# Optimization experiments

Measured on AMD Instinct MI355X. Metric: run time of the kernel, lower is better.

The kernel has to match this reference:

```python
import jax, jax.numpy as jnp
import numpy as np

# ---- model constants (match init_kwargs) ----
B, N, T, L = 16384, 32, 300, 1
DIM = 2                      # len(state_index)
DT = 1.0 / (T * L)           # dt = 1/(T*l)
STEPS = T * L                # Euler integration steps (time_steps = STEPS+1)
A_X = 1.0                    # canonical DMP phase constant
TAU = 1.0
HID = 64
OUT = N * DIM + DIM          # fc2_mean output size


def setup_inputs() -> dict:
    key = jax.random.key(0)
    ks = jax.random.split(key, 8)
    s = lambda i, shape, scale: jax.random.normal(ks[i], shape, jnp.float32) * scale
    inp = {
        "state": jax.random.normal(ks[0], (B, 3), jnp.float32),
        "fc1_w": s(1, (HID, 3), 0.3),
        "fc1_b": jnp.full((HID,), 0.1, jnp.float32),
        "fc2m_w": s(2, (OUT, HID), 0.1),
        "fc2m_b": jnp.full((OUT,), 0.1, jnp.float32),
        "sig_w": s(3, (DIM, HID), 0.1),
        "sig_b": jnp.zeros((DIM,), jnp.float32),
        "val_w": s(4, (DIM, HID), 0.1),
        "val_b": jnp.zeros((DIM,), jnp.float32),
    }
    # DMPParameters: gaussian RBF centers on exp-decayed phase, canonical widths
    c = jnp.exp(-A_X * jnp.linspace(0.0, 1.0, N))
    inp["dmp_c"] = c.astype(jnp.float32)
    inp["dmp_sigma2"] = (N ** 1.5 / c / A_X).astype(jnp.float32)
    return inp


def dmp_rollout(w, goal, y0, dy0, a_z, c, sigma2):
    """Euler rollout of DMP transformation system.
    w: [M,N] basis weights, goal/y0/dy0/a_z: [M] per-channel scalars.
    Returns Y, dY, ddY each [M, STEPS+1]."""
    z0 = dy0 * TAU
    b_z = a_z / 4.0

    def step(carry, _):
        x, y, z = carry
        x = x + (-A_X * x) * TAU * DT                       # phase update
        psi = jnp.exp(-0.5 * (x - c) ** 2 / sigma2)          # [N] gaussian RBF
        fx = (w @ psi) * x * (goal - y0) / jnp.sum(psi)      # [M] forcing term
        dz = a_z * (b_z * (goal - y) - z) + fx
        dy = z
        y = y + TAU * dy * DT
        z = z + TAU * dz * DT
        return (x, y, z), (y, dy * TAU, dz * TAU)

    _, (Ys, dYs, ddYs) = jax.lax.scan(
        step, (jnp.float32(1.0), y0, z0), None, length=STEPS)
    Y = jnp.concatenate([y0[None], Ys], axis=0).T            # [M, STEPS+1]
    dY = jnp.concatenate([dy0[None], dYs], axis=0).T
    ddY = jnp.concatenate([z0[None], ddYs], axis=0).T
    return Y, dY, ddY


def reference(state, fc1_w, fc1_b, fc2m_w, fc2m_b, sig_w, sig_b,
              val_w, val_b, dmp_c, dmp_sigma2):
    x = jnp.tanh(state @ fc1_w.T + fc1_b) * 0.1              # [B,64]
    y0 = state[:, :DIM].reshape(-1)                           # [M=B*DIM]
    dy0 = jnp.zeros_like(y0) + 0.01

    # value = fc2_value(x).repeat(1,T).view(-1,T,2).transpose(1,2) == broadcast over T
    v = x @ val_w.T + val_b                                   # [B,2]
    value = jnp.broadcast_to(v[:, :, None], (B, DIM, T))

    sigma = (jax.nn.sigmoid(x @ sig_w.T + sig_b) * 1.0 + 0.001).reshape(-1, DIM, 1)

    ndp_wg = x @ fc2m_w.T + fc2m_b                            # [B, 2N+2]
    goal = ndp_wg[:, :DIM].reshape(-1)                        # [M]
    w = ndp_wg[:, DIM:DIM * (N + 1)].reshape(-1, N)           # [M,N]
    a_z = jnp.clip(ndp_wg[:, -1], 0.5, 30.0)                  # learned a_z (az=True)
    a_z = jnp.broadcast_to(a_z[:, None], (B, DIM)).reshape(-1)

    Y, _, _ = dmp_rollout(w, goal, y0, dy0, a_z, dmp_c, dmp_sigma2)
    y = Y.reshape(B, DIM, -1)[:, :, ::L]                      # [B,2,T+1]
    a = y[:, :, 1:] - y[:, :, :-1]                            # [B,2,T]
    return (a, sigma, value)
```

## Files before the change

kernel.cpp:

```cpp
#include <hip/hip_runtime.h>
#include <hip/hip_bf16.h>

#define NB 32
#define TS 300
#define NBATCH 16384
#define DTF (1.0f/300.0f)
#define A_ELEMS (NBATCH*2*TS)

typedef __attribute__((ext_vector_type(8))) short bf16x8;
typedef __attribute__((ext_vector_type(4))) float f32x4;

static __device__ __forceinline__ ushort f2bf(float f) {
    union { __hip_bfloat16 h; ushort u; } cv;
    cv.h = __float2bfloat16(f);
    return cv.u;
}


__global__ __launch_bounds__(256) void k_head(
    const float* __restrict__ state,
    const float* __restrict__ fc1_w, const float* __restrict__ fc1_b,
    const float* __restrict__ fc2m_w, const float* __restrict__ fc2m_b,
    const float* __restrict__ sig_w, const float* __restrict__ sig_b,
    const float* __restrict__ val_w, const float* __restrict__ val_b,
    const float* __restrict__ dmp_c, const float* __restrict__ dmp_s2,
    float* __restrict__ sig_out, float* __restrict__ pbuf,
    ushort* __restrict__ wbuf16, uint4* __restrict__ wsPhi)
{
    const int tid = threadIdx.x;
    if (blockIdx.x == 256) {
        const float l2 = log2f(1.0f - DTF);
        for (int t = tid; t < 304; t += 256) {
            ushort row[NB];
            if (t < TS) {
                const float x = exp2f((float)(t + 1) * l2);
                float ps[NB]; float s = 0.0f;
                #pragma unroll
                for (int n = 0; n < NB; ++n) {
                    float d = x - dmp_c[n];
                    float p = __expf(-0.5f * d * d / dmp_s2[n]);
                    ps[n] = p; s += p;
                }
                const float inv = x / s;
                #pragma unroll
                for (int n = 0; n < NB; ++n) row[n] = f2bf(ps[n] * inv);
            } else {
                #pragma unroll
                for (int n = 0; n < NB; ++n) row[n] = 0;
            }
            #pragma unroll
            for (int g0 = 0; g0 < 4; ++g0) {
                union { ushort us[8]; uint4 v; } pk;
                #pragma unroll
                for (int e = 0; e < 8; ++e) pk.us[e] = row[g0*8 + e];
                wsPhi[(t >> 4)*64 + g0*16 + (t & 15)] = pk.v;
            }
        }
        return;
    }

    __shared__ uint4 bfr[640];
    __shared__ float f1s[64*4];
    __shared__ float biasl[80];
    __shared__ float hlds[4*16*68];
    __shared__ float ct[4*16*84];
    __shared__ float scl[4][16][2];

    const int wv  = tid >> 6;
    const int l   = tid & 63;
    const int b16 = l & 15;
    const int g   = l >> 4;

    for (int e = tid; e < 640; e += 256) {
        const int T = e >> 7, kk = (e >> 6) & 1, lane = e & 63;
        const int r = T*16 + (lane & 15);
        const int k0 = kk*32 + (lane >> 4)*8;
        union { ushort us[8]; uint4 v; } pk;
        if (r < 70) {
            const float* src = (r < 66) ? (fc2m_w + r*64 + k0)
                             : (r < 68) ? (sig_w + (r-66)*64 + k0)
                             : (val_w + (r-68)*64 + k0);
            #pragma unroll
            for (int i = 0; i < 8; ++i) pk.us[i] = f2bf(src[i]);
        } else {
            #pragma unroll
            for (int i = 0; i < 8; ++i) pk.us[i] = 0;
        }
        bfr[e] = pk.v;
    }
    if (tid < 64) {
        f1s[tid*4+0] = fc1_w[tid*3+0];
        f1s[tid*4+1] = fc1_w[tid*3+1];
        f1s[tid*4+2] = fc1_w[tid*3+2];
        f1s[tid*4+3] = fc1_b[tid];
    }
    if (tid < 80) biasl[tid] = (tid < 66) ? fc2m_b[tid] : (tid < 68) ? sig_b[tid-66]
                             : (tid < 70) ? val_b[tid-68] : 0.0f;
    __syncthreads();

    const int bbase = blockIdx.x*64 + wv*16;
    const int bglob = bbase + b16;
    const float s0 = state[bglob*3+0], s1 = state[bglob*3+1], s2 = state[bglob*3+2];

    float* hrow = hlds + wv*1088 + b16*68;
    #pragma unroll
    for (int i = 0; i < 16; ++i) {
        const int hid = g + 4*i;
        const float4 fw = *(const float4*)(f1s + hid*4);
        const float pre = fmaf(fw.x, s0, fmaf(fw.y, s1, fmaf(fw.z, s2, fw.w)));
        const float e = __expf(2.0f * pre);
        hrow[hid] = (1.0f - 2.0f/(e + 1.0f)) * 0.1f;
    }

    bf16x8 A0, A1;
    {
        const float* hr = hlds + wv*1088 + b16*68 + g*8;
        const float4 h0 = *(const float4*)(hr),      h1 = *(const float4*)(hr + 4);
        const float4 h2 = *(const float4*)(hr + 32), h3 = *(const float4*)(hr + 36);
        union { bf16x8 v; ushort u[8]; } p0, p1;
        p0.u[0]=f2bf(h0.x); p0.u[1]=f2bf(h0.y); p0.u[2]=f2bf(h0.z); p0.u[3]=f2bf(h0.w);
        p0.u[4]=f2bf(h1.x); p0.u[5]=f2bf(h1.y); p0.u[6]=f2bf(h1.z); p0.u[7]=f2bf(h1.w);
        p1.u[0]=f2bf(h2.x); p1.u[1]=f2bf(h2.y); p1.u[2]=f2bf(h2.z); p1.u[3]=f2bf(h2.w);
        p1.u[4]=f2bf(h3.x); p1.u[5]=f2bf(h3.y); p1.u[6]=f2bf(h3.z); p1.u[7]=f2bf(h3.w);
        A0 = p0.v; A1 = p1.v;
    }

    float* ctw = ct + wv*1344;
    const f32x4 zacc = {0.0f, 0.0f, 0.0f, 0.0f};
    #pragma unroll
    for (int T = 0; T < 5; ++T) {
        union { uint4 q; bf16x8 v; } B0, B1;
        B0.q = bfr[(T*2+0)*64 + l];
        B1.q = bfr[(T*2+1)*64 + l];
        f32x4 acc = __builtin_amdgcn_mfma_f32_16x16x32_bf16(A0, B0.v, zacc, 0, 0, 0);
        acc = __builtin_amdgcn_mfma_f32_16x16x32_bf16(A1, B1.v, acc, 0, 0, 0);
        const int r = T*16 + b16;
        const float bs = biasl[r];
        #pragma unroll
        for (int reg = 0; reg < 4; ++reg)
            ctw[(g*4 + reg)*84 + r] = acc[reg] + bs;
    }

    if (l < 32) {
        const int b = l & 15, d = l >> 4;
        const float goal = ctw[b*84 + d];
        const float y0 = state[(bbase + b)*3 + d];
        scl[wv][b][d] = DTF * (goal - y0);
    }

    uint* wout = (uint*)wbuf16;
    #pragma unroll 1
    for (int b = 0; b < 16; ++b) {
        if (l < 32) {
            const float2 wp = *(const float2*)(ctw + b*84 + 2 + 2*l);
            const float sc = scl[wv][b][l >> 4];
            wout[(bbase + b)*32 + l] =
                (uint)f2bf(wp.x * sc) | ((uint)f2bf(wp.y * sc) << 16);
        }
    }
    if (l < 16) {
        const float* cb = ctw + l*84;
        const float az = fminf(fmaxf(cb[65], 0.5f), 30.0f);
        const float y0 = state[(bbase + l)*3 + 0];
        *(float4*)(pbuf + ((bbase + l)*2 + 0)*4) = make_float4(cb[0], az, y0, cb[68]);
    } else if (l < 32) {
        const int b = l - 16;
        const float* cb = ctw + b*84;
        const float az = fminf(fmaxf(cb[65], 0.5f), 30.0f);
        const float y0 = state[(bbase + b)*3 + 1];
        *(float4*)(pbuf + ((bbase + b)*2 + 1)*4) = make_float4(cb[1], az, y0, cb[69]);
    } else if (l < 48) {
        const int b = l - 32;
        const float* cb = ctw + b*84;
        const float sg0 = 1.0f / (1.0f + __expf(-cb[66])) + 0.001f;
        const float sg1 = 1.0f / (1.0f + __expf(-cb[67])) + 0.001f;
        *(float2*)(sig_out + (bbase + b)*2) = make_float2(sg0, sg1);
    }
}

__global__ __launch_bounds__(384) void k_roll(
    const uint4* __restrict__ wsPhi, const float* __restrict__ pbuf,
    const ushort* __restrict__ wbuf16, float* __restrict__ a_out,
    float* __restrict__ v_out)
{
    const int tid = threadIdx.x;
    const int wv = tid >> 6;
    const int l  = tid & 63;

    if (wv >= 4) {
        const int vw = wv - 4;
        const int mbase = (blockIdx.x << 6) + (vw << 5);
        #pragma unroll 1
        for (int r = 0; r < 32; ++r) {
            const int mch = mbase + r;
            const float fv = pbuf[mch*4 + 3];
            float4* vrow = (float4*)(v_out + mch*TS);
            const float4 vq = make_float4(fv, fv, fv, fv);
            vrow[l] = vq;
            if (l < 11) vrow[64 + l] = vq;
        }
        return;
    }

    const int ch = l & 15;
    const int g  = l >> 4;
    const int m  = (blockIdx.x << 6) + (wv << 4) + ch;

    const float4 pp = *(const float4*)(pbuf + m*4);
    const float az = pp.y;
    const float Ac = (DTF * 0.25f) * az * az;
    const float OmB = fmaf(-DTF, az, 1.0f);
    const float c0 = Ac * pp.x;
    float y = pp.z;
    float z = 0.01f;
    const f32x4 cvec = {c0, c0, c0, c0};

    const bf16x8 wb = *(const bf16x8*)(wbuf16 + m*NB + g*8);
    const bf16x8* ap = (const bf16x8*)wsPhi;
    bf16x8 af = ap[l];

    float* aptr = a_out + m*TS + (g << 2);

    for (int c = 0; c < 19; ++c) {
        f32x4 facc = __builtin_amdgcn_mfma_f32_16x16x32_bf16(af, wb, cvec, 0, 0, 0);
        if (c < 18) af = ap[(c + 1)*64 + l];

        float F[16];
        #pragma unroll
        for (int q = 0; q < 4; ++q) {
            float a = facc[q], b = facc[q];
            asm volatile("v_permlane16_swap_b32 %0, %1" : "+v"(a), "+v"(b));
            float a2 = a, b2 = b;
            asm volatile("v_permlane32_swap_b32 %0, %1" : "+v"(a), "+v"(a2));
            asm volatile("v_permlane32_swap_b32 %0, %1" : "+v"(b), "+v"(b2));
            F[0*4+q] = a; F[1*4+q] = b; F[2*4+q] = a2; F[3*4+q] = b2;
        }

        float avq[4];
        #pragma unroll
        for (int i = 0; i < 16; ++i) {
            const float t2 = fmaf(-Ac, y, F[i]);
            if (g == (i >> 2)) avq[i & 3] = z;
            y = fmaf(DTF, z, y);
            z = fmaf(OmB, z, t2);
        }

        if ((c < 18) | (g < 3)) {
            *(float4*)aptr = make_float4(avq[0]*DTF, avq[1]*DTF, avq[2]*DTF, avq[3]*DTF);
        }
        aptr += 16;
    }
}

extern "C" void kernel_launch(void* const* d_in, const int* in_sizes, int n_in,
                              void* d_out, int out_size, void* d_ws, size_t ws_size,
                              hipStream_t stream) {
    (void)in_sizes; (void)n_in; (void)out_size; (void)ws_size;
    const float* state  = (const float*)d_in[0];
    const float* fc1_w  = (const float*)d_in[1];
    const float* fc1_b  = (const float*)d_in[2];
    const float* fc2m_w = (const float*)d_in[3];
    const float* fc2m_b = (const float*)d_in[4];
    const float* sig_w  = (const float*)d_in[5];
    const float* sig_b  = (const float*)d_in[6];
    const float* val_w  = (const float*)d_in[7];
    const float* val_b  = (const float*)d_in[8];
    const float* dmp_c  = (const float*)d_in[9];
    const float* dmp_s2 = (const float*)d_in[10];

    float* out     = (float*)d_out;
    float* a_out   = out;
    float* sig_out = out + A_ELEMS;
    float* v_out   = out + A_ELEMS + NBATCH*2;

    char* ws = (char*)d_ws;
    uint4*  wsPhi  = (uint4*)ws;
    float*  pbuf   = (float*)(ws + 32768);
    ushort* wbuf16 = (ushort*)(ws + 557056);

    k_head<<<dim3(257), dim3(256), 0, stream>>>(state, fc1_w, fc1_b, fc2m_w, fc2m_b,
                                                sig_w, sig_b, val_w, val_b,
                                                dmp_c, dmp_s2,
                                                sig_out, pbuf, wbuf16, wsPhi);
    k_roll<<<dim3(512), dim3(384), 0, stream>>>(wsPhi, pbuf, wbuf16, a_out, v_out);
}
```

Measured before the change: 27.96 us.

## Fuse head MLP and DMP rollout into one kernel with LDS-resident basis table

Merges the head kernel and the rollout kernel into a single 768-thread block. Each block computes the MLP head for its 64 batch rows, rebuilds the normalized RBF phase table in shared memory with two spare waves, and then runs the rollout and value broadcast for its own 128 channels after a block barrier. This removes the second kernel launch and the global round-trip of the basis table. In exchange every block recomputes the basis table, and the grid becomes 256 large blocks, which limits overlap and occupancy during the rollout.

After: 27.47 us. No clear change (-1.8%).

```diff
diff --git a/kernel.cpp b/kernel.cpp
--- a/kernel.cpp
+++ b/kernel.cpp
@@ -16,8 +16,7 @@
     return cv.u;
 }
 
-
-__global__ __launch_bounds__(256) void k_head(
+__global__ __launch_bounds__(768) void k_all(
     const float* __restrict__ state,
     const float* __restrict__ fc1_w, const float* __restrict__ fc1_b,
     const float* __restrict__ fc2m_w, const float* __restrict__ fc2m_b,
@@ -25,12 +24,50 @@
     const float* __restrict__ val_w, const float* __restrict__ val_b,
     const float* __restrict__ dmp_c, const float* __restrict__ dmp_s2,
     float* __restrict__ sig_out, float* __restrict__ pbuf,
-    ushort* __restrict__ wbuf16, uint4* __restrict__ wsPhi)
+    ushort* __restrict__ wbuf16,
+    float* __restrict__ a_out, float* __restrict__ v_out)
 {
+    __shared__ uint4 phiL[19*64];
+    __shared__ uint4 bfr[640];
+    __shared__ float f1s[64*4];
+    __shared__ float biasl[80];
+    __shared__ float hlds[4*16*68];
+    __shared__ float ct[4*16*84];
+    __shared__ float scl[4][16][2];
+
     const int tid = threadIdx.x;
-    if (blockIdx.x == 256) {
+    const int wv  = tid >> 6;
+    const int l   = tid & 63;
+
+    if (wv < 4) {
+        for (int e = tid; e < 640; e += 256) {
+            const int T = e >> 7, kk = (e >> 6) & 1, lane = e & 63;
+            const int r = T*16 + (lane & 15);
+            const int k0 = kk*32 + (lane >> 4)*8;
+            union { ushort us[8]; uint4 v; } pk;
+            if (r < 70) {
+                const float* src = (r < 66) ? (fc2m_w + r*64 + k0)
+                                 : (r < 68) ? (sig_w + (r-66)*64 + k0)
+                                 : (val_w + (r-68)*64 + k0);
+                #pragma unroll
+                for (int i = 0; i < 8; ++i) pk.us[i] = f2bf(src[i]);
+            } else {
+                #pragma unroll
+                for (int i = 0; i < 8; ++i) pk.us[i] = 0;
+            }
+            bfr[e] = pk.v;
+        }
+        if (tid < 64) {
+            f1s[tid*4+0] = fc1_w[tid*3+0];
+            f1s[tid*4+1] = fc1_w[tid*3+1];
+            f1s[tid*4+2] = fc1_w[tid*3+2];
+            f1s[tid*4+3] = fc1_b[tid];
+        }
+        if (tid < 80) biasl[tid] = (tid < 66) ? fc2m_b[tid] : (tid < 68) ? sig_b[tid-66]
+                                 : (tid < 70) ? val_b[tid-68] : 0.0f;
+    } else if (wv < 6) {
         const float l2 = log2f(1.0f - DTF);
-        for (int t = tid; t < 304; t += 256) {
+        for (int t = tid - 256; t < 304; t += 128) {
             ushort row[NB];
             if (t < TS) {
                 const float x = exp2f((float)(t + 1) * l2);
@@ -53,143 +90,148 @@
                 union { ushort us[8]; uint4 v; } pk;
                 #pragma unroll
                 for (int e = 0; e < 8; ++e) pk.us[e] = row[g0*8 + e];
-                wsPhi[(t >> 4)*64 + g0*16 + (t & 15)] = pk.v;
-            }
-        }
-        return;
+                phiL[(t >> 4)*64 + g0*16 + (t & 15)] = pk.v;
+            }
+        }
     }
-
-    __shared__ uint4 bfr[640];
-    __shared__ float f1s[64*4];
-    __shared__ float biasl[80];
-    __shared__ float hlds[4*16*68];
-    __shared__ float ct[4*16*84];
-    __shared__ float scl[4][16][2];
-
-    const int wv  = tid >> 6;
-    const int l   = tid & 63;
-    const int b16 = l & 15;
-    const int g   = l >> 4;
-
-    for (int e = tid; e < 640; e += 256) {
-        const int T = e >> 7, kk = (e >> 6) & 1, lane = e & 63;
-        const int r = T*16 + (lane & 15);
-        const int k0 = kk*32 + (lane >> 4)*8;
-        union { ushort us[8]; uint4 v; } pk;
-        if (r < 70) {
-            const float* src = (r < 66) ? (fc2m_w + r*64 + k0)
-                             : (r < 68) ? (sig_w + (r-66)*64 + k0)
-                             : (val_w + (r-68)*64 + k0);
-            #pragma unroll
-            for (int i = 0; i < 8; ++i) pk.us[i] = f2bf(src[i]);
-        } else {
-            #pragma unroll
-            for (int i = 0; i < 8; ++i) pk.us[i] = 0;
-        }
-        bfr[e] = pk.v;
+    __syncthreads();
+
+    if (wv < 4) {
+        const int b16 = l & 15;
+        const int g   = l >> 4;
+        const int bbase = blockIdx.x*64 + wv*16;
+        const int bglob = bbase + b16;
+        const float s0 = state[bglob*3+0], s1 = state[bglob*3+1], s2 = state[bglob*3+2];
+
+        float* hrow = hlds + wv*1088 + b16*68;
+        #pragma unroll
+        for (int i = 0; i < 16; ++i) {
+            const int hid = g + 4*i;
+            const float4 fw = *(const float4*)(f1s + hid*4);
+            const float pre = fmaf(fw.x, s0, fmaf(fw.y, s1, fmaf(fw.z, s2, fw.w)));
+            const float e = __expf(2.0f * pre);
+            hrow[hid] = (1.0f - 2.0f/(e + 1.0f)) * 0.1f;
+        }
+
+        bf16x8 A0, A1;
+        {
+            const float* hr = hlds + wv*1088 + b16*68 + g*8;
+            const float4 h0 = *(const float4*)(hr),      h1 = *(const float4*)(hr + 4);
+            const float4 h2 = *(const float4*)(hr + 32), h3 = *(const float4*)(hr + 36);
+            union { bf16x8 v; ushort u[8]; } p0, p1;
+            p0.u[0]=f2bf(h0.x); p0.u[1]=f2bf(h0.y); p0.u[2]=f2bf(h0.z); p0.u[3]=f2bf(h0.w);
+            p0.u[4]=f2bf(h1.x); p0.u[5]=f2bf(h1.y); p0.u[6]=f2bf(h1.z); p0.u[7]=f2bf(h1.w);
+            p1.u[0]=f2bf(h2.x); p1.u[1]=f2bf(h2.y); p1.u[2]=f2bf(h2.z); p1.u[3]=f2bf(h2.w);
+            p1.u[4]=f2bf(h3.x); p1.u[5]=f2bf(h3.y); p1.u[6]=f2bf(h3.z); p1.u[7]=f2bf(h3.w);
+            A0 = p0.v; A1 = p1.v;
+        }
+
+        float* ctw = ct + wv*1344;
+        const f32x4 zacc = {0.0f, 0.0f, 0.0f, 0.0f};
+        #pragma unroll
+        for (int T = 0; T < 5; ++T) {
+            union { uint4 q; bf16x8 v; } B0, B1;
+            B0.q = bfr[(T*2+0)*64 + l];
+            B1.q = bfr[(T*2+1)*64 + l];
+            f32x4 acc = __builtin_amdgcn_mfma_f32_16x16x32_bf16(A0, B0.v, zacc, 0, 0, 0);
+            acc = __builtin_amdgcn_mfma_f32_16x16x32_bf16(A1, B1.v, acc, 0, 0, 0);
+            const int r = T*16 + b16;
+            const float bs = biasl[r];
+            #pragma unroll
+            for (int reg = 0; reg < 4; ++reg)
+                ctw[(g*4 + reg)*84 + r] = acc[reg] + bs;
+        }
+
+        if (l < 32) {
+            const int b = l & 15, d = l >> 4;
+            const float goal = ctw[b*84 + d];
+            const float y0 = state[(bbase + b)*3 + d];
+            scl[wv][b][d] = DTF * (goal - y0);
+        }
+
+        uint* wout = (uint*)wbuf16;
+        #pragma unroll 1
+        for (int b = 0; b < 16; ++b) {
+            if (l < 32) {
+                const float2 wp = *(const float2*)(ctw + b*84 + 2 + 2*l);
+                const float sc = scl[wv][b][l >> 4];
+                wout[(bbase + b)*32 + l] =
+                    (uint)f2bf(wp.x * sc) | ((uint)f2bf(wp.y * sc) << 16);
+            }
+        }
+        if (l < 16) {
+            const float* cb = ctw + l*84;
+            const float az = fminf(fmaxf(cb[65], 0.5f), 30.0f);
+            const float y0 = state[(bbase + l)*3 + 0];
+            *(float4*)(pbuf + ((bbase + l)*2 + 0)*4) = make_float4(cb[0], az, y0, cb[68]);
+        } else if (l < 32) {
+            const int b = l - 16;
+            const float* cb = ctw + b*84;
+            const float az = fminf(fmaxf(cb[65], 0.5f), 30.0f);
+            const float y0 = state[(bbase + b)*3 + 1];
+            *(float4*)(pbuf + ((bbase + b)*2 + 1)*4) = make_float4(cb[1], az, y0, cb[69]);
+        } else if (l < 48) {
+            const int b = l - 32;
+            const float* cb = ctw + b*84;
+            const float sg0 = 1.0f / (1.0f + __expf(-cb[66])) + 0.001f;
+            const float sg1 = 1.0f / (1.0f + __expf(-cb[67])) + 0.001f;
+            *(float2*)(sig_out + (bbase + b)*2) = make_float2(sg0, sg1);
+        }
     }
-    if (tid < 64) {
-        f1s[tid*4+0] = fc1_w[tid*3+0];
-        f1s[tid*4+1] = fc1_w[tid*3+1];
-        f1s[tid*4+2] = fc1_w[tid*3+2];
-        f1s[tid*4+3] = fc1_b[tid];
-    }
-    if (tid < 80) biasl[tid] = (tid < 66) ? fc2m_b[tid] : (tid < 68) ? sig_b[tid-66]
-                             : (tid < 70) ? val_b[tid-68] : 0.0f;
     __syncthreads();
 
-    const int bbase = blockIdx.x*64 + wv*16;
-    const int bglob = bbase + b16;
-    const float s0 = state[bglob*3+0], s1 = state[bglob*3+1], s2 = state[bglob*3+2];
-
-    float* hrow = hlds + wv*1088 + b16*68;
-    #pragma unroll
-    for (int i = 0; i < 16; ++i) {
-        const int hid = g + 4*i;
-        const float4 fw = *(const float4*)(f1s + hid*4);
-        const float pre = fmaf(fw.x, s0, fmaf(fw.y, s1, fmaf(fw.z, s2, fw.w)));
-        const float e = __expf(2.0f * pre);
-        hrow[hid] = (1.0f - 2.0f/(e + 1.0f)) * 0.1f;
-    }
-
-    bf16x8 A0, A1;
-    {
-        const float* hr = hlds + wv*1088 + b16*68 + g*8;
-        const float4 h0 = *(const float4*)(hr),      h1 = *(const float4*)(hr + 4);
-        const float4 h2 = *(const float4*)(hr + 32), h3 = *(const float4*)(hr + 36);
-        union { bf16x8 v; ushort u[8]; } p0, p1;
-        p0.u[0]=f2bf(h0.x); p0.u[1]=f2bf(h0.y); p0.u[2]=f2bf(h0.z); p0.u[3]=f2bf(h0.w);
-        p0.u[4]=f2bf(h1.x); p0.u[5]=f2bf(h1.y); p0.u[6]=f2bf(h1.z); p0.u[7]=f2bf(h1.w);
-        p1.u[0]=f2bf(h2.x); p1.u[1]=f2bf(h2.y); p1.u[2]=f2bf(h2.z); p1.u[3]=f2bf(h2.w);
-        p1.u[4]=f2bf(h3.x); p1.u[5]=f2bf(h3.y); p1.u[6]=f2bf(h3.z); p1.u[7]=f2bf(h3.w);
-        A0 = p0.v; A1 = p1.v;
-    }
-
-    float* ctw = ct + wv*1344;
-    const f32x4 zacc = {0.0f, 0.0f, 0.0f, 0.0f};
-    #pragma unroll
-    for (int T = 0; T < 5; ++T) {
-        union { uint4 q; bf16x8 v; } B0, B1;
-        B0.q = bfr[(T*2+0)*64 + l];
-        B1.q = bfr[(T*2+1)*64 + l];
-        f32x4 acc = __builtin_amdgcn_mfma_f32_16x16x32_bf16(A0, B0.v, zacc, 0, 0, 0);
-        acc = __builtin_amdgcn_mfma_f32_16x16x32_bf16(A1, B1.v, acc, 0, 0, 0);
-        const int r = T*16 + b16;
-        const float bs = biasl[r];
-        #pragma unroll
-        for (int reg = 0; reg < 4; ++reg)
-            ctw[(g*4 + reg)*84 + r] = acc[reg] + bs;
-    }
-
-    if (l < 32) {
-        const int b = l & 15, d = l >> 4;
-        const float goal = ctw[b*84 + d];
-        const float y0 = state[(bbase + b)*3 + d];
-        scl[wv][b][d] = DTF * (goal - y0);
-    }
-
-    uint* wout = (uint*)wbuf16;
-    #pragma unroll 1
-    for (int b = 0; b < 16; ++b) {
-        if (l < 32) {
-            const float2 wp = *(const float2*)(ctw + b*84 + 2 + 2*l);
-            const float sc = scl[wv][b][l >> 4];
-            wout[(bbase + b)*32 + l] =
-                (uint)f2bf(wp.x * sc) | ((uint)f2bf(wp.y * sc) << 16);
-        }
-    }
-    if (l < 16) {
-        const float* cb = ctw + l*84;
-        const float az = fminf(fmaxf(cb[65], 0.5f), 30.0f);
-        const float y0 = state[(bbase + l)*3 + 0];
-        *(float4*)(pbuf + ((bbase + l)*2 + 0)*4) = make_float4(cb[0], az, y0, cb[68]);
-    } else if (l < 32) {
-        const int b = l - 16;
-        const float* cb = ctw + b*84;
-        const float az = fminf(fmaxf(cb[65], 0.5f), 30.0f);
-        const float y0 = state[(bbase + b)*3 + 1];
-        *(float4*)(pbuf + ((bbase + b)*2 + 1)*4) = make_float4(cb[1], az, y0, cb[69]);
-    } else if (l < 48) {
-        const int b = l - 32;
-        const float* cb = ctw + b*84;
-        const float sg0 = 1.0f / (1.0f + __expf(-cb[66])) + 0.001f;
-        const float sg1 = 1.0f / (1.0f + __expf(-cb[67])) + 0.001f;
-        *(float2*)(sig_out + (bbase + b)*2) = make_float2(sg0, sg1);
-    }
-}
-
-__global__ __launch_bounds__(384) void k_roll(
-    const uint4* __restrict__ wsPhi, const float* __restrict__ pbuf,
-    const ushort* __restrict__ wbuf16, float* __restrict__ a_out,
-    float* __restrict__ v_out)
-{
-    const int tid = threadIdx.x;
-    const int wv = tid >> 6;
-    const int l  = tid & 63;
-
-    if (wv >= 4) {
-        const int vw = wv - 4;
-        const int mbase = (blockIdx.x << 6) + (vw << 5);
+    if (wv < 8) {
+        const int ch = l & 15;
+        const int g  = l >> 4;
+        const int m  = (blockIdx.x << 7) + (wv << 4) + ch;
+
+        const float4 pp = *(const float4*)(pbuf + m*4);
+        const float az = pp.y;
+        const float Ac = (DTF * 0.25f) * az * az;
+        const float OmB = fmaf(-DTF, az, 1.0f);
+        const float c0 = Ac * pp.x;
+        float y = pp.z;
+        float z = 0.01f;
+        const f32x4 cvec = {c0, c0, c0, c0};
+
+        const bf16x8 wb = *(const bf16x8*)(wbuf16 + m*NB + g*8);
+        const bf16x8* ap = (const bf16x8*)phiL;
+        bf16x8 af = ap[l];
+
+        float* aptr = a_out + m*TS + (g << 2);
+
+        for (int c = 0; c < 19; ++c) {
+            f32x4 facc = __builtin_amdgcn_mfma_f32_16x16x32_bf16(af, wb, cvec, 0, 0, 0);
+            if (c < 18) af = ap[(c + 1)*64 + l];
+
+            float F[16];
+            #pragma unroll
+            for (int q = 0; q < 4; ++q) {
+                float a = facc[q], b = facc[q];
+                asm volatile("v_permlane16_swap_b32 %0, %1" : "+v"(a), "+v"(b));
+                float a2 = a, b2 = b;
+                asm volatile("v_permlane32_swap_b32 %0, %1" : "+v"(a), "+v"(a2));
+                asm volatile("v_permlane32_swap_b32 %0, %1" : "+v"(b), "+v"(b2));
+                F[0*4+q] = a; F[1*4+q] = b; F[2*4+q] = a2; F[3*4+q] = b2;
+            }
+
+            float avq[4];
+            #pragma unroll
+            for (int i = 0; i < 16; ++i) {
+                const float t2 = fmaf(-Ac, y, F[i]);
+                if (g == (i >> 2)) avq[i & 3] = z;
+                y = fmaf(DTF, z, y);
+                z = fmaf(OmB, z, t2);
+            }
+
+            if ((c < 18) | (g < 3)) {
+                *(float4*)aptr = make_float4(avq[0]*DTF, avq[1]*DTF, avq[2]*DTF, avq[3]*DTF);
+            }
+            aptr += 16;
+        }
+    } else {
+        const int vw = wv - 8;
+        const int mbase = (blockIdx.x << 7) + (vw << 5);
         #pragma unroll 1
         for (int r = 0; r < 32; ++r) {
             const int mch = mbase + r;
@@ -199,56 +241,6 @@
             vrow[l] = vq;
             if (l < 11) vrow[64 + l] = vq;
         }
-        return;
-    }
-
-    const int ch = l & 15;
-    const int g  = l >> 4;
-    const int m  = (blockIdx.x << 6) + (wv << 4) + ch;
-
-    const float4 pp = *(const float4*)(pbuf + m*4);
-    const float az = pp.y;
-    const float Ac = (DTF * 0.25f) * az * az;
-    const float OmB = fmaf(-DTF, az, 1.0f);
-    const float c0 = Ac * pp.x;
-    float y = pp.z;
-    float z = 0.01f;
-    const f32x4 cvec = {c0, c0, c0, c0};
-
-    const bf16x8 wb = *(const bf16x8*)(wbuf16 + m*NB + g*8);
-    const bf16x8* ap = (const bf16x8*)wsPhi;
-    bf16x8 af = ap[l];
-
-    float* aptr = a_out + m*TS + (g << 2);
-
-    for (int c = 0; c < 19; ++c) {
-        f32x4 facc = __builtin_amdgcn_mfma_f32_16x16x32_bf16(af, wb, cvec, 0, 0, 0);
-        if (c < 18) af = ap[(c + 1)*64 + l];
-
-        float F[16];
-        #pragma unroll
-        for (int q = 0; q < 4; ++q) {
-            float a = facc[q], b = facc[q];
-            asm volatile("v_permlane16_swap_b32 %0, %1" : "+v"(a), "+v"(b));
-            float a2 = a, b2 = b;
-            asm volatile("v_permlane32_swap_b32 %0, %1" : "+v"(a), "+v"(a2));
-            asm volatile("v_permlane32_swap_b32 %0, %1" : "+v"(b), "+v"(b2));
-            F[0*4+q] = a; F[1*4+q] = b; F[2*4+q] = a2; F[3*4+q] = b2;
-        }
-
-        float avq[4];
-        #pragma unroll
-        for (int i = 0; i < 16; ++i) {
-            const float t2 = fmaf(-Ac, y, F[i]);
-            if (g == (i >> 2)) avq[i & 3] = z;
-            y = fmaf(DTF, z, y);
-            z = fmaf(OmB, z, t2);
-        }
-
-        if ((c < 18) | (g < 3)) {
-            *(float4*)aptr = make_float4(avq[0]*DTF, avq[1]*DTF, avq[2]*DTF, avq[3]*DTF);
-        }
-        aptr += 16;
     }
 }
 
@@ -274,13 +266,11 @@
     float* v_out   = out + A_ELEMS + NBATCH*2;
 
     char* ws = (char*)d_ws;
-    uint4*  wsPhi  = (uint4*)ws;
     float*  pbuf   = (float*)(ws + 32768);
     ushort* wbuf16 = (ushort*)(ws + 557056);
 
-    k_head<<<dim3(257), dim3(256), 0, stream>>>(state, fc1_w, fc1_b, fc2m_w, fc2m_b,
-                                                sig_w, sig_b, val_w, val_b,
-                                                dmp_c, dmp_s2,
-                                                sig_out, pbuf, wbuf16, wsPhi);
-    k_roll<<<dim3(512), dim3(384), 0, stream>>>(wsPhi, pbuf, wbuf16, a_out, v_out);
+    k_all<<<dim3(256), dim3(768), 0, stream>>>(state, fc1_w, fc1_b, fc2m_w, fc2m_b,
+                                               sig_w, sig_b, val_w, val_b,
+                                               dmp_c, dmp_s2,
+                                               sig_out, pbuf, wbuf16, a_out, v_out);
 }
```
